# Optimization experiments

Hardware: AMD Instinct MI355X
Metric: run time of the kernel (lower is better)

The kernel has to match this reference:

```python
import jax, jax.numpy as jnp
import numpy as np

HEADS = 8
KV_HEADS = 4
HEAD_DIM = 256
HIDDEN = 2560
WINDOW = 1024          # sliding_window (layer is sliding: (0+1) % 6 != 0)
SCALE = 256.0 ** -0.5  # query_pre_attn_scalar ** -0.5
ROPE_BASE = 10000.0    # rope_local_base_freq for sliding layers
EPS = 1e-6
NEG = -1e30


def rms_norm(x, w, eps=EPS):
    # x: [..., D]; effective weight is (1 + param) per the RMSNorm module
    var = jnp.mean(x * x, axis=-1, keepdims=True)
    return x * jax.lax.rsqrt(var + eps) * w


def rope(x, base, offset):
    # x: [B, H, T, D]; rotate-half RoPE over the full head_dim
    T, D = x.shape[2], x.shape[3]
    half = D // 2
    pos = (offset + jnp.arange(T)).astype(jnp.float32)           # [T]
    inv_freq = base ** (-jnp.arange(half, dtype=jnp.float32) * 2.0 / D)  # [half]
    ang = pos[:, None] * inv_freq[None, :]                       # [T, half]
    cos, sin = jnp.cos(ang), jnp.sin(ang)
    x1, x2 = x[..., :half], x[..., half:]
    return jnp.concatenate([x1 * cos - x2 * sin, x2 * cos + x1 * sin], axis=-1)


def setup_inputs() -> dict:
    key = jax.random.key(0)
    ks = jax.random.split(key, 7)
    B, T, S = 2, 1024, 4096
    w_std = 0.02
    return {
        "x": jax.random.normal(ks[0], (B, T, HIDDEN), dtype=jnp.float32),
        "k_cache": jax.random.normal(ks[1], (B, KV_HEADS, S, HEAD_DIM), dtype=jnp.float32),
        "v_cache": jax.random.normal(ks[2], (B, KV_HEADS, S, HEAD_DIM), dtype=jnp.float32),
        "wq": jax.random.normal(ks[3], (HIDDEN, HEADS * HEAD_DIM), dtype=jnp.float32) * w_std,
        "wk": jax.random.normal(ks[4], (HIDDEN, KV_HEADS * HEAD_DIM), dtype=jnp.float32) * w_std,
        "wv": jax.random.normal(ks[5], (HIDDEN, KV_HEADS * HEAD_DIM), dtype=jnp.float32) * w_std,
        "wo": jax.random.normal(ks[6], (HEADS * HEAD_DIM, HIDDEN), dtype=jnp.float32) * w_std,
        "q_norm_w": jnp.zeros((HEAD_DIM,), dtype=jnp.float32),
        "k_norm_w": jnp.zeros((HEAD_DIM,), dtype=jnp.float32),
        "pos_offset": 2048,
        "cache_index": 2048,
    }


def reference(x, k_cache, v_cache, wq, wk, wv, wo, q_norm_w, k_norm_w, pos_offset, cache_index):
    B, T, _ = x.shape
    # QKV projections -> [B, H, T, D]
    q = (x @ wq).reshape(B, T, HEADS, HEAD_DIM).transpose(0, 2, 1, 3)
    k = (x @ wk).reshape(B, T, KV_HEADS, HEAD_DIM).transpose(0, 2, 1, 3)
    v = (x @ wv).reshape(B, T, KV_HEADS, HEAD_DIM).transpose(0, 2, 1, 3)
    # per-head RMSNorm (effective weight 1 + param)
    q = rms_norm(q, 1.0 + q_norm_w)
    k = rms_norm(k, 1.0 + k_norm_w)
    # RoPE with position offset
    q = rope(q, ROPE_BASE, pos_offset)
    k = rope(k, ROPE_BASE, pos_offset)
    # KV cache update at cache_index along the sequence axis
    k_new = jax.lax.dynamic_update_slice(k_cache, k, (0, 0, cache_index, 0))
    v_new = jax.lax.dynamic_update_slice(v_cache, v, (0, 0, cache_index, 0))
    S = k_new.shape[2]
    # sliding-window validity mask over cached keys (as in the module: shared over queries)
    idx = jnp.arange(S)
    valid = (idx < cache_index + T) & (idx >= cache_index + T - WINDOW)   # [S]
    # GQA attention: group queries over kv heads
    G = HEADS // KV_HEADS
    qg = q.reshape(B, KV_HEADS, G, T, HEAD_DIM)
    scores = jnp.einsum('bkgtd,bksd->bkgts', qg, k_new) * SCALE           # [B,KV,G,T,S]
    scores = jnp.where(valid[None, None, None, None, :], scores, NEG)
    p = jax.nn.softmax(scores, axis=-1)
    out = jnp.einsum('bkgts,bksd->bkgtd', p, v_new)                       # [B,KV,G,T,D]
    out = out.reshape(B, HEADS, T, HEAD_DIM).transpose(0, 2, 1, 3).reshape(B, T, HEADS * HEAD_DIM)
    return out @ wo, k_new, v_new
```

## Files before the change

### kernel.cpp

```cpp
#include <hip/hip_runtime.h>

typedef __bf16 bf16;
typedef __bf16 bf16x8 __attribute__((ext_vector_type(8)));
typedef __bf16 bf16x4 __attribute__((ext_vector_type(4)));
typedef float f32x4 __attribute__((ext_vector_type(4)));

#define MFMA16(a, b, c) __builtin_amdgcn_mfma_f32_16x16x32_bf16(a, b, c, 0, 0, 0)

#define GLL(lds, g)                                                    \
  __builtin_amdgcn_global_load_lds(                                    \
      (const __attribute__((address_space(1))) void*)(g),              \
      (__attribute__((address_space(3))) void*)(lds), 16, 0, 0)

__global__ __launch_bounds__(256) void prep_kernel(
    const float* __restrict__ kc, const float* __restrict__ vc,
    float* __restrict__ kout, float* __restrict__ vout,
    const int* __restrict__ p_ci, const float* __restrict__ x,
    bf16* __restrict__ xb, const float* __restrict__ wq,
    const float* __restrict__ wk, const float* __restrict__ wv,
    bf16* __restrict__ wqkv_t, const float* __restrict__ wo,
    bf16* __restrict__ wo_t) {
  const int blk = blockIdx.x;
  const int tid = threadIdx.x;
  if (blk >= 3840) {
    if (blk < 6400) {
      const long i = (long)(blk - 3840) * 512 + tid;
      const float4 v0 = ((const float4*)x)[i];
      const float4 v1 = ((const float4*)x)[i + 256];
      bf16x4 o0, o1;
      o0.x = (bf16)v0.x; o0.y = (bf16)v0.y; o0.z = (bf16)v0.z; o0.w = (bf16)v0.w;
      o1.x = (bf16)v1.x; o1.y = (bf16)v1.y; o1.z = (bf16)v1.z; o1.w = (bf16)v1.w;
      ((bf16x4*)xb)[i] = o0;
      ((bf16x4*)xb)[i + 256] = o1;
      return;
    }
    const int cb = blk - 6400;
    const int bk = cb >> 8;
    const int s0 = (cb & 255) * 16 + (tid >> 6) * 4;
    const int l = tid & 63;
    const int ci = *p_ci;
#pragma unroll
    for (int i = 0; i < 4; ++i) {
      const int s = s0 + i;
      if ((unsigned)(s - ci) < 1024u) continue;
      const long base = ((long)bk * 4096 + s) * 64 + l;
      ((float4*)kout)[base] = ((const float4*)kc)[base];
      ((float4*)vout)[base] = ((const float4*)vc)[base];
    }
    return;
  }
  __shared__ float tile[64][65];
  const float* src;
  int k0, n0, col, srcN, dstK;
  bf16* dst;
  if (blk < 2560) {
    const int idx = blk;
    k0 = (idx % 40) * 64; n0 = (idx / 40) * 64;
    dstK = 2560; dst = wqkv_t;
    if (n0 < 2048)      { src = wq; col = n0;        srcN = 2048; }
    else if (n0 < 3072) { src = wk; col = n0 - 2048; srcN = 1024; }
    else                { src = wv; col = n0 - 3072; srcN = 1024; }
  } else {
    const int idx = blk - 2560;
    k0 = (idx & 31) * 64; n0 = (idx >> 5) * 64;
    dstK = 2048; dst = wo_t; src = wo; col = n0; srcN = 2560;
  }
  {
    const int rf = tid >> 4, c4 = (tid & 15) * 4;
#pragma unroll
    for (int i = 0; i < 4; ++i) {
      const int r = i * 16 + rf;
      const float4 v = *(const float4*)(src + (long)(k0 + r) * srcN + col + c4);
      tile[r][c4] = v.x; tile[r][c4 + 1] = v.y;
      tile[r][c4 + 2] = v.z; tile[r][c4 + 3] = v.w;
    }
  }
  __syncthreads();
  {
    const int nf = tid >> 3, kcq = (tid & 7) * 8;
#pragma unroll
    for (int i = 0; i < 2; ++i) {
      const int nn = i * 32 + nf;
      bf16x8 o8;
#pragma unroll
      for (int j = 0; j < 8; ++j) o8[j] = (bf16)tile[kcq + j][nn];
      *(bf16x8*)(dst + (long)(n0 + nn) * dstK + k0 + kcq) = o8;
    }
  }
}

__global__ __launch_bounds__(256) void v_trans_kernel(const bf16* __restrict__ qkv,
                                                      const int* __restrict__ p_ci,
                                                      float* __restrict__ vout,
                                                      bf16* __restrict__ vt) {
  __shared__ float tile[32][33];
  const int s0 = blockIdx.x * 32, d0 = blockIdx.y * 32, bk = blockIdx.z;
  const int b = bk >> 2, kvh = bk & 3;
  const int ci = *p_ci;
  const int tx = threadIdx.x, ty = threadIdx.y;
#pragma unroll
  for (int i = 0; i < 4; ++i) {
    const int s = s0 + ty + i * 8;
    const float val =
        (float)qkv[(long)(b * 1024 + s) * 4096 + (12 + kvh) * 256 + d0 + tx];
    tile[ty + i * 8][tx] = val;
    vout[((long)bk * 4096 + ci + s) * 256 + d0 + tx] = val;
  }
  __syncthreads();
  bf16* dstb = vt + ((long)bk * 256 + d0) * 1024 + s0;
#pragma unroll
  for (int i = 0; i < 4; ++i)
    dstb[(long)(ty + i * 8) * 1024 + tx] = (bf16)tile[tx][ty + i * 8];
}

template <int BM, int BN, int K, int N, typename OutT>
__global__ __launch_bounds__(256) void gemm_kernel(const bf16* __restrict__ A,
                                                   const bf16* __restrict__ BT,
                                                   OutT* __restrict__ C) {
  __shared__ bf16 As[2 * BM * 32];
  __shared__ bf16 Bs[2 * BN * 32];
  const int bm = blockIdx.x, bn = blockIdx.y;
  const int tid = threadIdx.x;
  const int wave = tid >> 6, lane = tid & 63;
  const int quad = lane >> 4, l16 = lane & 15;
  constexpr int WM = BM / 2, WN = BN / 2;
  constexpr int MI = WM / 16, NI = WN / 16;
  const int wm = (wave & 1) * WM, wn = (wave >> 1) * WN;
  f32x4 acc[MI][NI] = {};
  const int srow = tid >> 2;
  const int sslot = tid & 3;
  const bf16* Ag = A + (long)(bm * BM) * K;
  const bf16* Bg = BT + (long)(bn * BN) * K;
  auto stage = [&](int buf, int k0) {
#pragma unroll
    for (int i = 0; i < BM / 64; ++i) {
      const int r = i * 64 + srow;
      const int cc = (sslot - (r >> 1)) & 3;
      GLL(As + buf * BM * 32 + (i * 256 + wave * 64) * 8,
          Ag + (long)r * K + k0 + cc * 8);
    }
#pragma unroll
    for (int i = 0; i < BN / 64; ++i) {
      const int r = i * 64 + srow;
      const int cc = (sslot - (r >> 1)) & 3;
      GLL(Bs + buf * BN * 32 + (i * 256 + wave * 64) * 8,
          Bg + (long)r * K + k0 + cc * 8);
    }
  };
  stage(0, 0);
  int buf = 0;
  for (int k0 = 0; k0 < K; k0 += 32) {
    __syncthreads();
    if (k0 + 32 < K) stage(buf ^ 1, k0 + 32);
    const bf16* Ab = As + buf * BM * 32;
    const bf16* Bb = Bs + buf * BN * 32;
    bf16x8 af[MI], bfr[NI];
#pragma unroll
    for (int mi = 0; mi < MI; ++mi) {
      const int r = wm + mi * 16 + l16;
      af[mi] = *(const bf16x8*)(Ab + r * 32 + (((quad + (r >> 1)) & 3) * 8));
    }
#pragma unroll
    for (int ni = 0; ni < NI; ++ni) {
      const int r = wn + ni * 16 + l16;
      bfr[ni] = *(const bf16x8*)(Bb + r * 32 + (((quad + (r >> 1)) & 3) * 8));
    }
#pragma unroll
    for (int mi = 0; mi < MI; ++mi)
#pragma unroll
      for (int ni = 0; ni < NI; ++ni)
        acc[mi][ni] = MFMA16(af[mi], bfr[ni], acc[mi][ni]);
    buf ^= 1;
  }
  const int crow = bm * BM + wm + quad * 4;
  const int ccol = bn * BN + wn + l16;
#pragma unroll
  for (int mi = 0; mi < MI; ++mi)
#pragma unroll
    for (int ni = 0; ni < NI; ++ni)
#pragma unroll
      for (int r = 0; r < 4; ++r)
        C[(long)(crow + mi * 16 + r) * N + ccol + ni * 16] = (OutT)acc[mi][ni][r];
}

__global__ __launch_bounds__(384) void normrope_kernel(
    const bf16* __restrict__ qkv, const float* __restrict__ qw,
    const float* __restrict__ kw, const int* __restrict__ p_pos,
    const int* __restrict__ p_ci, float* __restrict__ kout,
    bf16* __restrict__ q_bf, bf16* __restrict__ k_bf) {
  const int bt = blockIdx.x;
  const int t = bt & 1023, b = bt >> 10;
  const int wave = threadIdx.x >> 6;
  const int lane = threadIdx.x & 63;
  const int half = lane >> 5;
  const int l32 = lane & 31;
  const int slot = wave * 2 + half;
  const int d0 = l32 * 8;
  const bf16x8 v8 = *(const bf16x8*)(qkv + (long)bt * 4096 + slot * 256 + d0);
  float v[8], ss = 0.0f;
#pragma unroll
  for (int j = 0; j < 8; ++j) {
    v[j] = (float)v8[j];
    ss += v[j] * v[j];
  }
#pragma unroll
  for (int i = 1; i < 32; i <<= 1) ss += __shfl_xor(ss, i);
  const float rstd = rsqrtf(ss * (1.0f / 256.0f) + 1e-6f);
  const bool isq = slot < 8;
  const float* wp = isq ? qw : kw;
  const float4 w0 = *(const float4*)(wp + d0);
  const float4 w1 = *(const float4*)(wp + d0 + 4);
  float nv[8];
  nv[0] = v[0] * rstd * (1.0f + w0.x); nv[1] = v[1] * rstd * (1.0f + w0.y);
  nv[2] = v[2] * rstd * (1.0f + w0.z); nv[3] = v[3] * rstd * (1.0f + w0.w);
  nv[4] = v[4] * rstd * (1.0f + w1.x); nv[5] = v[5] * rstd * (1.0f + w1.y);
  nv[6] = v[6] * rstd * (1.0f + w1.z); nv[7] = v[7] * rstd * (1.0f + w1.w);
  float pv[8];
#pragma unroll
  for (int j = 0; j < 8; ++j) pv[j] = __shfl_xor(nv[j], 16);
  const float pt = (float)(*p_pos + t);
  const int e0 = (l32 & 15) * 8;
  float outv[8];
#pragma unroll
  for (int j = 0; j < 8; ++j) {
    const float inv_freq = exp2f((float)(e0 + j) * -0.10381025296522976f);
    float rev = pt * inv_freq * 0.15915494309189535f;
    rev = rev - floorf(rev);
    const float sn = __builtin_amdgcn_sinf(rev);
    const float cs = __builtin_amdgcn_cosf(rev);
    outv[j] = (d0 < 128) ? nv[j] * cs - pv[j] * sn : nv[j] * cs + pv[j] * sn;
  }
  bf16x8 ob;
#pragma unroll
  for (int j = 0; j < 8; ++j) ob[j] = (bf16)outv[j];
  if (isq) {
    *(bf16x8*)(q_bf + ((long)(b * 8 + slot) * 1024 + t) * 256 + d0) = ob;
  } else {
    const int kh = slot - 8;
    const int ci = *p_ci;
    *(bf16x8*)(k_bf + ((long)(b * 4 + kh) * 1024 + t) * 256 + d0) = ob;
    float4 f0, f1;
    f0.x = outv[0]; f0.y = outv[1]; f0.z = outv[2]; f0.w = outv[3];
    f1.x = outv[4]; f1.y = outv[5]; f1.z = outv[6]; f1.w = outv[7];
    float* kg = kout + ((long)(b * 4 + kh) * 4096 + ci + t) * 256 + d0;
    *(float4*)(kg) = f0;
    *(float4*)(kg + 4) = f1;
  }
}

__global__ __launch_bounds__(256) void attn_kernel(const bf16* __restrict__ q_bf,
                                                   const bf16* __restrict__ k_bf,
                                                   const bf16* __restrict__ vt_bf,
                                                   bf16* __restrict__ attn) {
  __shared__ bf16 Ks[64 * 256];
  __shared__ bf16 Vs[256 * 64];
  __shared__ bf16 Ps[64 * 72];
  const int qt = blockIdx.x, h = blockIdx.y, b = blockIdx.z;
  const int kvh = h >> 1;
  const int tid = threadIdx.x;
  const int wave = tid >> 6, lane = tid & 63, quad = lane >> 4, l16 = lane & 15;
  bf16x8 qf[8];
  const bf16* qg =
      q_bf + ((long)(b * 8 + h) * 1024 + qt * 64 + wave * 16 + l16) * 256 + quad * 8;
#pragma unroll
  for (int i = 0; i < 8; ++i) qf[i] = *(const bf16x8*)(qg + i * 32);
  f32x4 o[16] = {};
  float m_r[4] = {-1e30f, -1e30f, -1e30f, -1e30f};
  float l_r[4] = {0.f, 0.f, 0.f, 0.f};
  const float sfac = 0.0625f * 1.44269504088896f;
  const bf16* kgb = k_bf + (long)(b * 4 + kvh) * 1024 * 256;
  const bf16* vgb = vt_bf + (long)(b * 4 + kvh) * 256 * 1024;
  const int krow = tid >> 5, kccp = tid & 31;
  const int kcc = kccp ^ (krow & 7);
  const int vrow0 = tid >> 3, vccp = tid & 7;
  for (int st = 0; st < 16; ++st) {
    __syncthreads();
#pragma unroll
    for (int i = 0; i < 8; ++i) {
      GLL(Ks + (i * 256 + wave * 64) * 8,
          kgb + (long)(st * 64 + krow + i * 8) * 256 + kcc * 8);
    }
#pragma unroll
    for (int i = 0; i < 8; ++i) {
      const int vr = vrow0 + i * 32;
      GLL(Vs + (i * 256 + wave * 64) * 8,
          vgb + (long)vr * 1024 + st * 64 + (vccp ^ (vr & 7)) * 8);
    }
    __syncthreads();
    f32x4 sacc[4] = {};
#pragma unroll
    for (int kk = 0; kk < 8; ++kk) {
#pragma unroll
      for (int ni = 0; ni < 4; ++ni) {
        const int r = ni * 16 + l16;
        bf16x8 kf = *(const bf16x8*)(Ks + r * 256 + (((kk * 4 + quad) ^ (r & 7)) * 8));
        sacc[ni] = MFMA16(qf[kk], kf, sacc[ni]);
      }
    }
    float alpha_r[4];
#pragma unroll
    for (int r = 0; r < 4; ++r) {
      float s0 = sacc[0][r] * sfac, s1 = sacc[1][r] * sfac;
      float s2 = sacc[2][r] * sfac, s3 = sacc[3][r] * sfac;
      float mx = fmaxf(fmaxf(s0, s1), fmaxf(s2, s3));
#pragma unroll
      for (int dd = 1; dd < 16; dd <<= 1) mx = fmaxf(mx, __shfl_xor(mx, dd));
      float mnew = fmaxf(m_r[r], mx);
      float al = exp2f(m_r[r] - mnew);
      m_r[r] = mnew;
      alpha_r[r] = al;
      float p0 = exp2f(s0 - mnew), p1 = exp2f(s1 - mnew);
      float p2 = exp2f(s2 - mnew), p3 = exp2f(s3 - mnew);
      float rs = p0 + p1 + p2 + p3;
#pragma unroll
      for (int dd = 1; dd < 16; dd <<= 1) rs += __shfl_xor(rs, dd);
      l_r[r] = l_r[r] * al + rs;
      const int prow = (wave * 16 + quad * 4 + r) * 72;
      Ps[prow + l16] = (bf16)p0;
      Ps[prow + 16 + l16] = (bf16)p1;
      Ps[prow + 32 + l16] = (bf16)p2;
      Ps[prow + 48 + l16] = (bf16)p3;
    }
#pragma unroll
    for (int n2 = 0; n2 < 16; ++n2) {
      f32x4 tv = o[n2];
      tv.x *= alpha_r[0]; tv.y *= alpha_r[1]; tv.z *= alpha_r[2]; tv.w *= alpha_r[3];
      o[n2] = tv;
    }
    bf16x8 pf0 = *(const bf16x8*)(Ps + (wave * 16 + l16) * 72 + quad * 8);
    bf16x8 pf1 = *(const bf16x8*)(Ps + (wave * 16 + l16) * 72 + 32 + quad * 8);
#pragma unroll
    for (int n2 = 0; n2 < 16; ++n2) {
      const int r = n2 * 16 + l16;
      bf16x8 vf0 = *(const bf16x8*)(Vs + r * 64 + ((quad ^ (r & 7)) * 8));
      o[n2] = MFMA16(pf0, vf0, o[n2]);
      bf16x8 vf1 = *(const bf16x8*)(Vs + r * 64 + (((4 + quad) ^ (r & 7)) * 8));
      o[n2] = MFMA16(pf1, vf1, o[n2]);
    }
  }
  float inv_l[4];
#pragma unroll
  for (int r = 0; r < 4; ++r) inv_l[r] = 1.0f / l_r[r];
  bf16* og = attn + ((long)(b * 1024 + qt * 64 + wave * 16 + quad * 4)) * 2048 +
             h * 256 + l16;
#pragma unroll
  for (int n2 = 0; n2 < 16; ++n2)
#pragma unroll
    for (int r = 0; r < 4; ++r)
      og[(long)r * 2048 + n2 * 16] = (bf16)(o[n2][r] * inv_l[r]);
}

extern "C" void kernel_launch(void* const* d_in, const int* in_sizes, int n_in,
                              void* d_out, int out_size, void* d_ws, size_t ws_size,
                              hipStream_t stream) {
  const float* x = (const float*)d_in[0];
  const float* k_cache = (const float*)d_in[1];
  const float* v_cache = (const float*)d_in[2];
  const float* wq = (const float*)d_in[3];
  const float* wk = (const float*)d_in[4];
  const float* wv = (const float*)d_in[5];
  const float* wo = (const float*)d_in[6];
  const float* qnw = (const float*)d_in[7];
  const float* knw = (const float*)d_in[8];
  const int* p_pos = (const int*)d_in[9];
  const int* p_ci = (const int*)d_in[10];

  float* out0 = (float*)d_out;
  float* kout = out0 + (long)2 * 1024 * 2560;
  float* vout = kout + (long)2 * 4 * 4096 * 256;

  char* w = (char*)d_ws;
  bf16* x_bf = (bf16*)(w);
  bf16* wqkv_t = (bf16*)(w + 10485760);
  bf16* wo_t = (bf16*)(w + 31457280);
  bf16* qkv = (bf16*)(w + 41943040);
  bf16* q_bf = (bf16*)(w + 58720256);
  bf16* k_bf = (bf16*)(w + 67108864);
  bf16* vt_bf = (bf16*)(w + 71303168);
  bf16* attn_b = (bf16*)(w + 75497472);

  prep_kernel<<<8448, 256, 0, stream>>>(k_cache, v_cache, kout, vout, p_ci, x,
                                        x_bf, wq, wk, wv, wqkv_t, wo, wo_t);

  gemm_kernel<128, 128, 2560, 4096, bf16>
      <<<dim3(16, 32), 256, 0, stream>>>(x_bf, wqkv_t, qkv);

  dim3 tb(32, 8);
  v_trans_kernel<<<dim3(32, 8, 8), tb, 0, stream>>>(qkv, p_ci, vout, vt_bf);

  normrope_kernel<<<2048, 384, 0, stream>>>(qkv, qnw, knw, p_pos, p_ci,
                                            kout, q_bf, k_bf);

  attn_kernel<<<dim3(16, 8, 2), 256, 0, stream>>>(q_bf, k_bf, vt_bf, attn_b);

  gemm_kernel<64, 128, 2048, 2560, float>
      <<<dim3(32, 20), 256, 0, stream>>>(attn_b, wo_t, out0);
}
```

Before: 401.5 us.

## Double-buffer K/V tiles in attention kernel with async LDS prefetch

The attention kernel now keeps two LDS buffers for K and V. It issues the global-to-LDS loads for the next tile before computing on the current one, waiting only on the older loads via vmcnt. This is meant to hide global memory latency behind the QK and PV MFMA work. In exchange, LDS use doubles to about 136KB per block, which cuts occupancy to one block per CU. The barriers after the raw s_waitcnt also rely on no other global loads being in flight inside the loop.

```diff
diff --git a/kernel.cpp b/kernel.cpp
--- a/kernel.cpp
+++ b/kernel.cpp
@@ -252,8 +252,8 @@
                                                    const bf16* __restrict__ k_bf,
                                                    const bf16* __restrict__ vt_bf,
                                                    bf16* __restrict__ attn) {
-  __shared__ bf16 Ks[64 * 256];
-  __shared__ bf16 Vs[256 * 64];
+  __shared__ bf16 Ks[2][64 * 256];
+  __shared__ bf16 Vs[2][256 * 64];
   __shared__ bf16 Ps[64 * 72];
   const int qt = blockIdx.x, h = blockIdx.y, b = blockIdx.z;
   const int kvh = h >> 1;
@@ -273,27 +273,38 @@
   const int krow = tid >> 5, kccp = tid & 31;
   const int kcc = kccp ^ (krow & 7);
   const int vrow0 = tid >> 3, vccp = tid & 7;
-  for (int st = 0; st < 16; ++st) {
-    __syncthreads();
+  auto stage = [&](int sb, int st) {
 #pragma unroll
     for (int i = 0; i < 8; ++i) {
-      GLL(Ks + (i * 256 + wave * 64) * 8,
+      GLL(&Ks[sb][(i * 256 + wave * 64) * 8],
           kgb + (long)(st * 64 + krow + i * 8) * 256 + kcc * 8);
     }
 #pragma unroll
     for (int i = 0; i < 8; ++i) {
       const int vr = vrow0 + i * 32;
-      GLL(Vs + (i * 256 + wave * 64) * 8,
+      GLL(&Vs[sb][(i * 256 + wave * 64) * 8],
           vgb + (long)vr * 1024 + st * 64 + (vccp ^ (vr & 7)) * 8);
     }
-    __syncthreads();
+  };
+  stage(0, 0);
+  int sb = 0;
+  for (int st = 0; st < 16; ++st) {
+    if (st < 15) {
+      stage(sb ^ 1, st + 1);
+      asm volatile("s_waitcnt vmcnt(16)" ::: "memory");
+    } else {
+      asm volatile("s_waitcnt vmcnt(0)" ::: "memory");
+    }
+    __builtin_amdgcn_s_barrier();
+    const bf16* Kb = Ks[sb];
+    const bf16* Vb = Vs[sb];
     f32x4 sacc[4] = {};
 #pragma unroll
     for (int kk = 0; kk < 8; ++kk) {
 #pragma unroll
       for (int ni = 0; ni < 4; ++ni) {
         const int r = ni * 16 + l16;
-        bf16x8 kf = *(const bf16x8*)(Ks + r * 256 + (((kk * 4 + quad) ^ (r & 7)) * 8));
+        bf16x8 kf = *(const bf16x8*)(Kb + r * 256 + (((kk * 4 + quad) ^ (r & 7)) * 8));
         sacc[ni] = MFMA16(qf[kk], kf, sacc[ni]);
       }
     }
@@ -332,11 +343,13 @@
 #pragma unroll
     for (int n2 = 0; n2 < 16; ++n2) {
       const int r = n2 * 16 + l16;
-      bf16x8 vf0 = *(const bf16x8*)(Vs + r * 64 + ((quad ^ (r & 7)) * 8));
+      bf16x8 vf0 = *(const bf16x8*)(Vb + r * 64 + ((quad ^ (r & 7)) * 8));
       o[n2] = MFMA16(pf0, vf0, o[n2]);
-      bf16x8 vf1 = *(const bf16x8*)(Vs + r * 64 + (((4 + quad) ^ (r & 7)) * 8));
+      bf16x8 vf1 = *(const bf16x8*)(Vb + r * 64 + (((4 + quad) ^ (r & 7)) * 8));
       o[n2] = MFMA16(pf1, vf1, o[n2]);
     }
+    __builtin_amdgcn_s_barrier();
+    sb ^= 1;
   }
   float inv_l[4];
 #pragma unroll
```

New measurement: 385.5 us. -4.0%, faster.
